# Kernel tuning notes

Hardware: AMD Instinct MI355X
Metric: run time of the kernel (lower is better)

Reference implementation:

```python
import jax, jax.numpy as jnp
import numpy as np

B, S, D, H = 2, 2048, 1024, 16
HD = D // H


def setup_inputs() -> dict:
    key = jax.random.key(0)
    ks = jax.random.split(key, 9)
    std = 0.02
    return {
        "x": jax.random.normal(ks[0], (B, S, D), dtype=jnp.float32),
        "wq": jax.random.normal(ks[1], (D, D), dtype=jnp.float32) * std,
        "bq": jnp.zeros((D,), dtype=jnp.float32),
        "wk": jax.random.normal(ks[2], (D, D), dtype=jnp.float32) * std,
        "bk": jnp.zeros((D,), dtype=jnp.float32),
        "wv": jax.random.normal(ks[3], (D, D), dtype=jnp.float32) * std,
        "bv": jnp.zeros((D,), dtype=jnp.float32),
        "wo": jax.random.normal(ks[4], (D, D), dtype=jnp.float32) * std,
        "bo": jnp.zeros((D,), dtype=jnp.float32),
    }


def reference(x, wq, bq, wk, bk, wv, bv, wo, bo):
    bsz, seq_len, d_model = x.shape
    # projections: torch Linear computes x @ W.T + b with W of shape (out, in)
    q = (x @ wq.T + bq).reshape(bsz, seq_len, H, HD).transpose(0, 2, 1, 3)  # bhsd
    k = (x @ wk.T + bk).reshape(bsz, seq_len, H, HD).transpose(0, 2, 1, 3)
    v = (x @ wv.T + bv).reshape(bsz, seq_len, H, HD).transpose(0, 2, 1, 3)
    scale = HD ** -0.5
    scores = jnp.einsum("bhqd,bhkd->bhqk", q, k) * scale  # [B,H,S,S]
    causal = jnp.tril(jnp.ones((seq_len, seq_len), dtype=bool))
    scores = jnp.where(causal[None, None], scores, -jnp.inf)
    attn = jax.nn.softmax(scores, axis=-1)
    ctx = jnp.einsum("bhqk,bhkd->bhqd", attn, v)
    ctx = ctx.transpose(0, 2, 1, 3).reshape(bsz, seq_len, d_model)
    return ctx @ wo.T + bo
```

## Files before the change

kernel.cpp:

```cpp
#include <hip/hip_runtime.h>
#include <hip/hip_bf16.h>

#define B_  2
#define S_  2048
#define D_  1024
#define H_  16
#define HD_ 64
#define M_  (B_ * S_)

typedef __bf16 bf16;
typedef __bf16 bf16x4 __attribute__((ext_vector_type(4)));
typedef __bf16 bf16x8 __attribute__((ext_vector_type(8)));
typedef float  f32x4  __attribute__((ext_vector_type(4)));
typedef unsigned int uint;

__device__ __forceinline__ bf16x8 ld8g(const bf16* p) { return *(const bf16x8*)p; }

#define GLL(g, l) __builtin_amdgcn_global_load_lds( \
    (const __attribute__((address_space(1))) void*)(g), \
    (__attribute__((address_space(3))) void*)(l), 16, 0, 0)

#define SWZ(row, byteoff) (((row) * 128) + ((byteoff) ^ (((row) & 7) << 4)))

__global__ __launch_bounds__(256) void convert_kernel(
    const float* __restrict__ x,  const float* __restrict__ wq,
    const float* __restrict__ wk, const float* __restrict__ wv,
    const float* __restrict__ wo,
    bf16* __restrict__ xb,  bf16* __restrict__ wqb, bf16* __restrict__ wkb,
    bf16* __restrict__ wvb, bf16* __restrict__ wob)
{
    const int seg = blockIdx.y;
    const float* src;
    bf16* dst;
    if (seg < 4)      { src = x  + (long)seg * 1048576; dst = xb  + (long)seg * 1048576; }
    else if (seg == 4){ src = wq; dst = wqb; }
    else if (seg == 5){ src = wk; dst = wkb; }
    else if (seg == 6){ src = wv; dst = wvb; }
    else              { src = wo; dst = wob; }
    const long i = ((long)blockIdx.x * 256 + threadIdx.x) * 8;
    float4 a = *(const float4*)(src + i);
    float4 b = *(const float4*)(src + i + 4);
    bf16x8 r;
    r[0] = (bf16)a.x; r[1] = (bf16)a.y; r[2] = (bf16)a.z; r[3] = (bf16)a.w;
    r[4] = (bf16)b.x; r[5] = (bf16)b.y; r[6] = (bf16)b.z; r[7] = (bf16)b.w;
    *(bf16x8*)(dst + i) = r;
}

__device__ __forceinline__ void gemm_acc_bk32(
    const bf16* __restrict__ A, const bf16* __restrict__ Bt,
    f32x4 (&acc)[4][4])
{
    __shared__ bf16 As[128 * 32];
    __shared__ bf16 Bs[128 * 32];

    const int tid  = threadIdx.x;
    const int wave = tid >> 6;
    const int lane = tid & 63;
    const int quad = lane >> 4;
    const int l15  = lane & 15;
    const int wr   = (wave >> 1) * 64;
    const int wc   = (wave & 1) * 64;
    const int m0   = blockIdx.y * 128;
    const int n0   = blockIdx.x * 128;

    const int sr = wave * 16 + (lane >> 2);
    const int sc = (lane & 3) * 8;
    const bf16* Ag = A  + (long)(m0 + sr) * D_ + sc;
    const bf16* Bg = Bt + (long)(n0 + sr) * D_ + sc;
    bf16* lA = As + wave * 512;
    bf16* lB = Bs + wave * 512;

    for (int k0 = 0; k0 < D_; k0 += 32) {
        __syncthreads();
        GLL(Ag + k0,             lA);
        GLL(Ag + 64 * D_ + k0,   lA + 64 * 32);
        GLL(Bg + k0,             lB);
        GLL(Bg + 64 * D_ + k0,   lB + 64 * 32);
        __syncthreads();

        bf16x8 af[4], bfr[4];
        for (int mi = 0; mi < 4; mi++)
            af[mi] = *(const bf16x8*)&As[(wr + mi * 16 + l15) * 32 + quad * 8];
        for (int ni = 0; ni < 4; ni++)
            bfr[ni] = *(const bf16x8*)&Bs[(wc + ni * 16 + l15) * 32 + quad * 8];

        for (int mi = 0; mi < 4; mi++)
            for (int ni = 0; ni < 4; ni++)
                acc[mi][ni] = __builtin_amdgcn_mfma_f32_16x16x32_bf16(
                    af[mi], bfr[ni], acc[mi][ni], 0, 0, 0);
    }
}

__global__ __launch_bounds__(256) void gemm_qkv(
    const bf16* __restrict__ xb,
    const bf16* __restrict__ wqb, const bf16* __restrict__ wkb, const bf16* __restrict__ wvb,
    const float* __restrict__ bq, const float* __restrict__ bk, const float* __restrict__ bv,
    bf16* __restrict__ qb, bf16* __restrict__ kb, bf16* __restrict__ vt)
{
    const bf16*  Bt   = (blockIdx.z == 0) ? wqb : (blockIdx.z == 1) ? wkb : wvb;
    const float* bias = (blockIdx.z == 0) ? bq  : (blockIdx.z == 1) ? bk  : bv;

    f32x4 acc[4][4] = {};
    gemm_acc_bk32(xb, Bt, acc);

    const int lane = threadIdx.x & 63;
    const int wave = threadIdx.x >> 6;
    const int quad = lane >> 4;
    const int l15  = lane & 15;
    const int wr   = (wave >> 1) * 64;
    const int wc   = (wave & 1) * 64;
    const int m0   = blockIdx.y * 128;
    const int n0   = blockIdx.x * 128;

    if (blockIdx.z < 2) {
        bf16* Cout = (blockIdx.z == 0) ? qb : kb;
        for (int ni = 0; ni < 4; ni++) {
            const int col = n0 + wc + ni * 16 + l15;
            const float bv = bias[col];
            for (int mi = 0; mi < 4; mi++) {
                const int rowb = m0 + wr + mi * 16 + quad * 4;
                for (int r = 0; r < 4; r++)
                    Cout[(long)(rowb + r) * D_ + col] = (bf16)(acc[mi][ni][r] + bv);
            }
        }
    } else {
        for (int ni = 0; ni < 4; ni++) {
            const int col = n0 + wc + ni * 16 + l15;
            const float bv = bias[col];
            const int h = col >> 6, hd = col & (HD_ - 1);
            for (int mi = 0; mi < 4; mi++) {
                const int rowb = m0 + wr + mi * 16 + quad * 4;
                const int b = rowb >> 11;
                const int s0 = rowb & (S_ - 1);
                bf16x4 v4;
                for (int r = 0; r < 4; r++) v4[r] = (bf16)(acc[mi][ni][r] + bv);
                *(bf16x4*)&vt[(((long)(b * H_ + h)) * HD_ + hd) * S_ + s0] = v4;
            }
        }
    }
}

__global__ __launch_bounds__(256) void gemm_out(
    const bf16* __restrict__ cb, const bf16* __restrict__ wob,
    const float* __restrict__ bo, float* __restrict__ out)
{
    __shared__ bf16 As[64 * 32];
    __shared__ bf16 Bs[128 * 32];

    const int tid  = threadIdx.x;
    const int wave = tid >> 6;
    const int lane = tid & 63;
    const int quad = lane >> 4;
    const int l15  = lane & 15;
    const int wr   = (wave >> 1) * 32;
    const int wc   = (wave & 1) * 64;
    const int m0   = blockIdx.y * 64;
    const int n0   = blockIdx.x * 128;

    const int sr = tid >> 2;
    const int scg = (tid & 3) * 8;
    const bf16* Ag = cb  + (long)(m0 + sr) * D_ + scg;
    const bf16* Bg = wob + (long)(n0 + sr) * D_ + scg;
    bf16* lA = As + wave * 512;
    bf16* lB = Bs + wave * 512;

    f32x4 acc[2][4] = {};
    for (int k0 = 0; k0 < D_; k0 += 32) {
        __syncthreads();
        GLL(Ag + k0,            lA);
        GLL(Bg + k0,            lB);
        GLL(Bg + 64 * D_ + k0,  lB + 64 * 32);
        __syncthreads();

        bf16x8 af[2], bfr[4];
        for (int mi = 0; mi < 2; mi++)
            af[mi] = *(const bf16x8*)&As[(wr + mi * 16 + l15) * 32 + quad * 8];
        for (int ni = 0; ni < 4; ni++)
            bfr[ni] = *(const bf16x8*)&Bs[(wc + ni * 16 + l15) * 32 + quad * 8];

        for (int mi = 0; mi < 2; mi++)
            for (int ni = 0; ni < 4; ni++)
                acc[mi][ni] = __builtin_amdgcn_mfma_f32_16x16x32_bf16(
                    af[mi], bfr[ni], acc[mi][ni], 0, 0, 0);
    }

    for (int ni = 0; ni < 4; ni++) {
        const int col = n0 + wc + ni * 16 + l15;
        const float bv = bo[col];
        for (int mi = 0; mi < 2; mi++) {
            const int rowb = m0 + wr + mi * 16 + quad * 4;
            for (int r = 0; r < 4; r++)
                out[(long)(rowb + r) * D_ + col] = acc[mi][ni][r] + bv;
        }
    }
}

__global__ __launch_bounds__(512, 4) void attn_kernel(
    const bf16* __restrict__ Q, const bf16* __restrict__ K,
    const bf16* __restrict__ vt, bf16* __restrict__ ctx)
{
    __shared__ bf16 Ks[2][64 * 64];
    __shared__ bf16 Vt[2][64 * 64];

    const int tid  = threadIdx.x;
    const int wave = tid >> 6;
    const int lane = tid & 63;
    const int quad = lane >> 4;
    const int l15  = lane & 15;
    const int bh   = blockIdx.y;
    const int qt   = (blockIdx.y < 16) ? blockIdx.x : (15 - (int)blockIdx.x);
    const int b    = bh >> 4, h = bh & 15;
    const long base = ((long)b * S_) * D_ + h * HD_;
    const bf16* Kg  = K + base;
    const bf16* Vth = vt + (long)bh * HD_ * S_;

    char* K0 = (char*)&Ks[0][0]; char* K1 = (char*)&Ks[1][0];
    char* V0 = (char*)&Vt[0][0]; char* V1 = (char*)&Vt[1][0];

    const int r0 = tid >> 3;
    const int c0 = (tid & 7) * 8;
    const int cB = (tid & 7) * 16;
    const int pr = (r0 & 32) + ((r0 >> 2) & 1) * 16 + ((r0 >> 3) & 3) * 4 + (r0 & 3);

    const int qw   = qt * 128 + wave * 16;
    const int qrow = qw + l15;
    const bf16* Qr = Q + base + (long)qrow * D_;
    bf16x8 qf0 = ld8g(&Qr[quad * 8]);
    bf16x8 qf1 = ld8g(&Qr[quad * 8 + 32]);

    float l_i = 0.f;
    f32x4 o_acc[4] = {};

    auto process_tile = [&](int kbase, int buf) {
        if (kbase > qw + 15) return;
        const char* Kb = buf ? K1 : K0;
        const char* Vb = buf ? V1 : V0;

        f32x4 sc[4];
        __builtin_amdgcn_s_setprio(1);
        #pragma unroll
        for (int kt = 0; kt < 4; kt++) {
            bf16x8 a0 = *(const bf16x8*)(Kb + SWZ(kt * 16 + l15, quad * 16));
            bf16x8 a1 = *(const bf16x8*)(Kb + SWZ(kt * 16 + l15, quad * 16 + 64));
            f32x4 z = {};
            z = __builtin_amdgcn_mfma_f32_16x16x32_bf16(a0, qf0, z, 0, 0, 0);
            z = __builtin_amdgcn_mfma_f32_16x16x32_bf16(a1, qf1, z, 0, 0, 0);
            sc[kt] = z;
        }
        __builtin_amdgcn_s_setprio(0);

        float sum = 0.f;
        if (kbase + 63 <= qw) {
            #pragma unroll
            for (int kt = 0; kt < 4; kt++)
                #pragma unroll
                for (int r = 0; r < 4; r++) {
                    const float p = __expf(sc[kt][r] * 0.125f);
                    sc[kt][r] = p;
                    sum += p;
                }
        } else {
            #pragma unroll
            for (int kt = 0; kt < 4; kt++)
                #pragma unroll
                for (int r = 0; r < 4; r++) {
                    const int kg = kbase + (kt >> 1) * 32 + quad * 8 + (kt & 1) * 4 + r;
                    const float p = (kg <= qrow) ? __expf(sc[kt][r] * 0.125f) : 0.f;
                    sc[kt][r] = p;
                    sum += p;
                }
        }
        sum += __shfl_xor(sum, 16, 64);
        sum += __shfl_xor(sum, 32, 64);
        l_i += sum;

        union { bf16 hh[8]; bf16x8 v; } pa0, pa1;
        #pragma unroll
        for (int r = 0; r < 4; r++) {
            pa0.hh[r]     = (bf16)sc[0][r];
            pa0.hh[r + 4] = (bf16)sc[1][r];
            pa1.hh[r]     = (bf16)sc[2][r];
            pa1.hh[r + 4] = (bf16)sc[3][r];
        }

        __builtin_amdgcn_s_setprio(1);
        #pragma unroll
        for (int ni = 0; ni < 4; ni++) {
            bf16x8 av0 = *(const bf16x8*)(Vb + SWZ(ni * 16 + l15, quad * 16));
            bf16x8 av1 = *(const bf16x8*)(Vb + SWZ(ni * 16 + l15, quad * 16 + 64));
            o_acc[ni] = __builtin_amdgcn_mfma_f32_16x16x32_bf16(av0, pa0.v, o_acc[ni], 0, 0, 0);
            o_acc[ni] = __builtin_amdgcn_mfma_f32_16x16x32_bf16(av1, pa1.v, o_acc[ni], 0, 0, 0);
        }
        __builtin_amdgcn_s_setprio(0);
    };

    bf16x8 kA = ld8g(Kg + (long)r0 * D_ + c0);
    bf16x8 wA = ld8g(Vth + (long)r0 * S_ + c0);
    bf16x8 kB = ld8g(Kg + (long)(64 + r0) * D_ + c0);
    bf16x8 wB = ld8g(Vth + (long)r0 * S_ + 64 + c0);

    const int njt = 2 * qt + 2;
    for (int j = 0; j < njt; j += 2) {
        __syncthreads();
        *(bf16x8*)(K0 + SWZ(pr, cB)) = kA;
        *(bf16x8*)(V0 + SWZ(r0, cB)) = wA;
        *(bf16x8*)(K1 + SWZ(pr, cB)) = kB;
        *(bf16x8*)(V1 + SWZ(r0, cB)) = wB;
        if (j + 2 < njt) {
            kA = ld8g(Kg + (long)((j + 2) * 64 + r0) * D_ + c0);
            wA = ld8g(Vth + (long)r0 * S_ + (j + 2) * 64 + c0);
            kB = ld8g(Kg + (long)((j + 3) * 64 + r0) * D_ + c0);
            wB = ld8g(Vth + (long)r0 * S_ + (j + 3) * 64 + c0);
        }
        __syncthreads();
        process_tile(j * 64, 0);
        process_tile(j * 64 + 64, 1);
    }

    __syncthreads();
    char* epi = (char*)&Ks[0][0] + wave * 2048;
    const float inv = 1.f / l_i;
    #pragma unroll
    for (int ni = 0; ni < 4; ni++) {
        union { uint2 u; bf16 hh[4]; } pk;
        pk.hh[0] = (bf16)(o_acc[ni][0] * inv);
        pk.hh[1] = (bf16)(o_acc[ni][1] * inv);
        pk.hh[2] = (bf16)(o_acc[ni][2] * inv);
        pk.hh[3] = (bf16)(o_acc[ni][3] * inv);
        *(uint2*)(epi + SWZ(l15, ni * 32 + quad * 8)) = pk.u;
    }
    __asm__ volatile("s_waitcnt lgkmcnt(0)" ::: "memory");
    __builtin_amdgcn_sched_barrier(0);
    #pragma unroll
    for (int round = 0; round < 2; round++) {
        const int rowq = (lane >> 3) + round * 8;
        bf16x8 val = *(const bf16x8*)(epi + SWZ(rowq, (lane & 7) * 16));
        const int q_g = qt * 128 + wave * 16 + rowq;
        *(bf16x8*)&ctx[base + (long)q_g * D_ + (lane & 7) * 8] = val;
    }
}

extern "C" void kernel_launch(void* const* d_in, const int* in_sizes, int n_in,
                              void* d_out, int out_size, void* d_ws, size_t ws_size,
                              hipStream_t stream)
{
    const float* x  = (const float*)d_in[0];
    const float* wq = (const float*)d_in[1];
    const float* bq = (const float*)d_in[2];
    const float* wk = (const float*)d_in[3];
    const float* bk = (const float*)d_in[4];
    const float* wv = (const float*)d_in[5];
    const float* bv = (const float*)d_in[6];
    const float* wo = (const float*)d_in[7];
    const float* bo = (const float*)d_in[8];
    float* out = (float*)d_out;

    const long NX = (long)M_ * D_;
    const long NW = (long)D_ * D_;
    bf16* xb  = (bf16*)d_ws;
    bf16* wqb = xb  + NX;
    bf16* wkb = wqb + NW;
    bf16* wvb = wkb + NW;
    bf16* wob = wvb + NW;
    bf16* qb  = wob + NW;
    bf16* kb  = qb  + NX;
    bf16* vt  = kb  + NX;
    bf16* cb  = xb;

    dim3 blk(256, 1, 1);

    convert_kernel<<<dim3(512, 8), blk, 0, stream>>>(
        x, wq, wk, wv, wo, xb, wqb, wkb, wvb, wob);

    gemm_qkv<<<dim3(8, 32, 3), blk, 0, stream>>>(
        xb, wqb, wkb, wvb, bq, bk, bv, qb, kb, vt);

    attn_kernel<<<dim3(16, 32), dim3(512, 1, 1), 0, stream>>>(qb, kb, vt, cb);

    gemm_out<<<dim3(8, 64), blk, 0, stream>>>(cb, wob, bo, out);
}
```

Before: 177.6 us.

## Shrink attention blocks to 64 query rows and double-buffer K/V tiles

The attention kernel now uses 256-thread blocks covering 64 query rows (1024 blocks instead of 512), which gives more parallelism and finer causal load balance. The K/V loading changes from staging two tiles per step to a one-tile-ahead double buffer. The next tile's global loads are issued before the current tile is computed and written to the other LDS buffer afterwards, so there is one barrier per tile. Each K/V tile is now loaded by more blocks, which raises global/L2 traffic.

```diff
diff --git a/kernel.cpp b/kernel.cpp
--- a/kernel.cpp
+++ b/kernel.cpp
@@ -195,7 +195,7 @@
     }
 }
 
-__global__ __launch_bounds__(512, 4) void attn_kernel(
+__global__ __launch_bounds__(256, 4) void attn_kernel(
     const bf16* __restrict__ Q, const bf16* __restrict__ K,
     const bf16* __restrict__ vt, bf16* __restrict__ ctx)
 {
@@ -208,7 +208,7 @@
     const int quad = lane >> 4;
     const int l15  = lane & 15;
     const int bh   = blockIdx.y;
-    const int qt   = (blockIdx.y < 16) ? blockIdx.x : (15 - (int)blockIdx.x);
+    const int qt   = (blockIdx.y < 16) ? blockIdx.x : (31 - (int)blockIdx.x);
     const int b    = bh >> 4, h = bh & 15;
     const long base = ((long)b * S_) * D_ + h * HD_;
     const bf16* Kg  = K + base;
@@ -220,9 +220,9 @@
     const int r0 = tid >> 3;
     const int c0 = (tid & 7) * 8;
     const int cB = (tid & 7) * 16;
-    const int pr = (r0 & 32) + ((r0 >> 2) & 1) * 16 + ((r0 >> 3) & 3) * 4 + (r0 & 3);
-
-    const int qw   = qt * 128 + wave * 16;
+    const int pr = ((r0 >> 2) & 1) * 16 + ((r0 >> 3) & 3) * 4 + (r0 & 3);
+
+    const int qw   = qt * 64 + wave * 16;
     const int qrow = qw + l15;
     const bf16* Qr = Q + base + (long)qrow * D_;
     bf16x8 qf0 = ld8g(&Qr[quad * 8]);
@@ -294,27 +294,36 @@
         __builtin_amdgcn_s_setprio(0);
     };
 
-    bf16x8 kA = ld8g(Kg + (long)r0 * D_ + c0);
-    bf16x8 wA = ld8g(Vth + (long)r0 * S_ + c0);
-    bf16x8 kB = ld8g(Kg + (long)(64 + r0) * D_ + c0);
-    bf16x8 wB = ld8g(Vth + (long)r0 * S_ + 64 + c0);
-
-    const int njt = 2 * qt + 2;
-    for (int j = 0; j < njt; j += 2) {
-        __syncthreads();
-        *(bf16x8*)(K0 + SWZ(pr, cB)) = kA;
-        *(bf16x8*)(V0 + SWZ(r0, cB)) = wA;
-        *(bf16x8*)(K1 + SWZ(pr, cB)) = kB;
-        *(bf16x8*)(V1 + SWZ(r0, cB)) = wB;
-        if (j + 2 < njt) {
-            kA = ld8g(Kg + (long)((j + 2) * 64 + r0) * D_ + c0);
-            wA = ld8g(Vth + (long)r0 * S_ + (j + 2) * 64 + c0);
-            kB = ld8g(Kg + (long)((j + 3) * 64 + r0) * D_ + c0);
-            wB = ld8g(Vth + (long)r0 * S_ + (j + 3) * 64 + c0);
-        }
-        __syncthreads();
-        process_tile(j * 64, 0);
-        process_tile(j * 64 + 64, 1);
+    bf16x8 kA0 = ld8g(Kg + (long)r0 * D_ + c0);
+    bf16x8 kA1 = ld8g(Kg + (long)(r0 + 32) * D_ + c0);
+    bf16x8 wA0 = ld8g(Vth + (long)r0 * S_ + c0);
+    bf16x8 wA1 = ld8g(Vth + (long)(r0 + 32) * S_ + c0);
+    *(bf16x8*)(K0 + SWZ(pr,      cB)) = kA0;
+    *(bf16x8*)(K0 + SWZ(pr + 32, cB)) = kA1;
+    *(bf16x8*)(V0 + SWZ(r0,      cB)) = wA0;
+    *(bf16x8*)(V0 + SWZ(r0 + 32, cB)) = wA1;
+    __syncthreads();
+
+    const int njt = qt + 1;
+    for (int j = 0; j < njt; ++j) {
+        const int cur = j & 1;
+        const bool more = (j + 1 < njt);
+        if (more) {
+            kA0 = ld8g(Kg + (long)((j + 1) * 64 + r0) * D_ + c0);
+            kA1 = ld8g(Kg + (long)((j + 1) * 64 + r0 + 32) * D_ + c0);
+            wA0 = ld8g(Vth + (long)r0 * S_ + (j + 1) * 64 + c0);
+            wA1 = ld8g(Vth + (long)(r0 + 32) * S_ + (j + 1) * 64 + c0);
+        }
+        process_tile(j * 64, cur);
+        if (more) {
+            char* Kd = cur ? K0 : K1;
+            char* Vd = cur ? V0 : V1;
+            *(bf16x8*)(Kd + SWZ(pr,      cB)) = kA0;
+            *(bf16x8*)(Kd + SWZ(pr + 32, cB)) = kA1;
+            *(bf16x8*)(Vd + SWZ(r0,      cB)) = wA0;
+            *(bf16x8*)(Vd + SWZ(r0 + 32, cB)) = wA1;
+            __syncthreads();
+        }
     }
 
     __syncthreads();
@@ -335,7 +344,7 @@
     for (int round = 0; round < 2; round++) {
         const int rowq = (lane >> 3) + round * 8;
         bf16x8 val = *(const bf16x8*)(epi + SWZ(rowq, (lane & 7) * 16));
-        const int q_g = qt * 128 + wave * 16 + rowq;
+        const int q_g = qt * 64 + wave * 16 + rowq;
         *(bf16x8*)&ctx[base + (long)q_g * D_ + (lane & 7) * 8] = val;
     }
 }
@@ -375,7 +384,7 @@
     gemm_qkv<<<dim3(8, 32, 3), blk, 0, stream>>>(
         xb, wqb, wkb, wvb, bq, bk, bv, qb, kb, vt);
 
-    attn_kernel<<<dim3(16, 32), dim3(512, 1, 1), 0, stream>>>(qb, kb, vt, cb);
+    attn_kernel<<<dim3(32, 32), blk, 0, stream>>>(qb, kb, vt, cb);
 
     gemm_out<<<dim3(8, 64), blk, 0, stream>>>(cb, wob, bo, out);
 }
```

Measured after the change: 185.7 us. +4.6%, slower.

## Stream K/V tiles via direct global-to-LDS loads with per-tile double buffering

Applied to the files above, without the earlier changes.

Replaces the register-staged K and V tile loads with global_load_lds async copies straight into shared memory. Global reads are pre-swizzled so the existing LDS layout is kept. The loop now advances one 64-key tile per iteration and prefetches the next tile into the other buffer while the current one is computed. This removes register pressure and the explicit LDS stores, but adds one barrier per tile instead of one per two tiles. Correctness depends on the swizzle and row permutation matching the old layout, and on the barrier placement covering completion of the async loads.

```diff
diff --git a/kernel.cpp b/kernel.cpp
--- a/kernel.cpp
+++ b/kernel.cpp
@@ -217,10 +217,17 @@
     char* K0 = (char*)&Ks[0][0]; char* K1 = (char*)&Ks[1][0];
     char* V0 = (char*)&Vt[0][0]; char* V1 = (char*)&Vt[1][0];
 
-    const int r0 = tid >> 3;
-    const int c0 = (tid & 7) * 8;
-    const int cB = (tid & 7) * 16;
-    const int pr = (r0 & 32) + ((r0 >> 2) & 1) * 16 + ((r0 >> 3) & 3) * 4 + (r0 & 3);
+    const int rho  = wave * 8 + (lane >> 3);
+    const int chnk = lane & 7;
+    const int scol = ((chnk ^ (rho & 7)) * 8);
+    const int gK = (rho & 32) + ((rho >> 3) & 1) * 16 + ((rho >> 2) & 1) * 8
+                 + ((rho >> 4) & 1) * 4 + (rho & 3);
+    const bf16* KgL = Kg  + (long)gK  * D_ + scol;
+    const bf16* VgL = Vth + (long)rho * S_ + scol;
+    bf16* Kw0 = (bf16*)(K0 + wave * 1024);
+    bf16* Vw0 = (bf16*)(V0 + wave * 1024);
+    bf16* Kw1 = (bf16*)(K1 + wave * 1024);
+    bf16* Vw1 = (bf16*)(V1 + wave * 1024);
 
     const int qw   = qt * 128 + wave * 16;
     const int qrow = qw + l15;
@@ -294,30 +301,21 @@
         __builtin_amdgcn_s_setprio(0);
     };
 
-    bf16x8 kA = ld8g(Kg + (long)r0 * D_ + c0);
-    bf16x8 wA = ld8g(Vth + (long)r0 * S_ + c0);
-    bf16x8 kB = ld8g(Kg + (long)(64 + r0) * D_ + c0);
-    bf16x8 wB = ld8g(Vth + (long)r0 * S_ + 64 + c0);
+    GLL(KgL, Kw0);
+    GLL(VgL, Vw0);
+    __syncthreads();
 
     const int njt = 2 * qt + 2;
-    for (int j = 0; j < njt; j += 2) {
-        __syncthreads();
-        *(bf16x8*)(K0 + SWZ(pr, cB)) = kA;
-        *(bf16x8*)(V0 + SWZ(r0, cB)) = wA;
-        *(bf16x8*)(K1 + SWZ(pr, cB)) = kB;
-        *(bf16x8*)(V1 + SWZ(r0, cB)) = wB;
-        if (j + 2 < njt) {
-            kA = ld8g(Kg + (long)((j + 2) * 64 + r0) * D_ + c0);
-            wA = ld8g(Vth + (long)r0 * S_ + (j + 2) * 64 + c0);
-            kB = ld8g(Kg + (long)((j + 3) * 64 + r0) * D_ + c0);
-            wB = ld8g(Vth + (long)r0 * S_ + (j + 3) * 64 + c0);
-        }
-        __syncthreads();
-        process_tile(j * 64, 0);
-        process_tile(j * 64 + 64, 1);
-    }
-
-    __syncthreads();
+    for (int j = 0; j < njt; ++j) {
+        const int cur = j & 1;
+        if (j + 1 < njt) {
+            GLL(KgL + (long)(j + 1) * 64 * D_, cur ? Kw0 : Kw1);
+            GLL(VgL + (j + 1) * 64,            cur ? Vw0 : Vw1);
+        }
+        process_tile(j * 64, cur);
+        __syncthreads();
+    }
+
     char* epi = (char*)&Ks[0][0] + wave * 2048;
     const float inv = 1.f / l_i;
     #pragma unroll
```

After: 177.8 us. Within noise of the previous version (+0.1%).
